# Optimization experiments

Measured on AMD Instinct MI355X. Metric: run time of the kernel, lower is better.

Reference implementation:

```python
import jax, jax.numpy as jnp
import numpy as np

HID, INP = 128, 320
C = HID + INP  # 448


def _fake_quant_w(w):
    # brevitas Int8WeightPerTensorFloat-style symmetric per-tensor fake quant (STE forward)
    scale = jnp.maximum(jnp.max(jnp.abs(w)), 1e-8) / 127.0
    q = jnp.clip(jnp.round(w / scale), -128, 127) * scale
    return w + jax.lax.stop_gradient(q - w)


def _dwconv(x, w, b):
    # depthwise 3x3, SAME padding; w: [C,1,3,3]
    y = jax.lax.conv_general_dilated(x, _fake_quant_w(w), (1, 1), 'SAME',
                                     dimension_numbers=('NCHW', 'OIHW', 'NCHW'),
                                     feature_group_count=x.shape[1])
    return y + b[None, :, None, None]


def _pwconv(x, w, b):
    # pointwise 1x1; w: [O,C,1,1]
    y = jax.lax.conv_general_dilated(x, _fake_quant_w(w), (1, 1), 'SAME',
                                     dimension_numbers=('NCHW', 'OIHW', 'NCHW'))
    return y + b[None, :, None, None]


def setup_inputs() -> dict:
    key = jax.random.key(0)
    ks = jax.random.split(key, 16)
    B, H, W = 8, 64, 128
    d = {
        'h': jax.random.normal(ks[0], (B, HID, H, W), jnp.float32),
        'x': jax.random.normal(ks[1], (B, INP, H, W), jnp.float32),
    }
    i = 2
    for g in ('z', 'r', 'q'):
        d[f'wd{g}'] = jax.random.normal(ks[i], (C, 1, 3, 3), jnp.float32) * 0.1; i += 1
        d[f'bd{g}'] = jax.random.normal(ks[i], (C,), jnp.float32) * 0.01; i += 1
        d[f'wp{g}'] = jax.random.normal(ks[i], (HID, C, 1, 1), jnp.float32) * 0.05; i += 1
        d[f'bp{g}'] = jax.random.normal(ks[i], (HID,), jnp.float32) * 0.01; i += 1
    return d


def reference(h, x, wdz, bdz, wpz, bpz, wdr, bdr, wpr, bpr, wdq, bdq, wpq, bpq):
    hx = jnp.concatenate([h, x], axis=1)  # [B, 448, H, W]
    z = jax.nn.sigmoid(_pwconv(_dwconv(hx, wdz, bdz), wpz, bpz))
    r = jax.nn.sigmoid(_pwconv(_dwconv(hx, wdr, bdr), wpr, bpr))
    rhx = jnp.concatenate([r * h, x], axis=1)
    q = jnp.tanh(_pwconv(_dwconv(rhx, wdq, bdq), wpq, bpq))
    return (1.0 - z) * h + z * q
```

## Files before the change

### kernel.cpp

```cpp
#include <hip/hip_runtime.h>
#include <hip/hip_bf16.h>

#define BB  8
#define HIDC 128
#define INPC 320
#define CC  448
#define HH  64
#define WWI 128
#define HW  8192
#define NT_PER_B 512
#define KG  56

using bf16   = __hip_bfloat16;
using bf16x8 = __attribute__((ext_vector_type(8))) __bf16;
using bf16x4 = __attribute__((ext_vector_type(4))) __bf16;
using bf16x2 = __attribute__((ext_vector_type(2))) __bf16;
using f32x4  = __attribute__((ext_vector_type(4))) float;
using f32x2  = __attribute__((ext_vector_type(2))) float;

__device__ __forceinline__ float b2f(bf16 v) { return __bfloat162float(v); }
__device__ __forceinline__ bf16  f2b(float v) { return __float2bfloat16(v); }

__device__ __forceinline__ void load2(const float* p, float& v0, float& v1) {
  f32x2 t = *reinterpret_cast<const f32x2*>(p);
  v0 = t[0]; v1 = t[1];
}
__device__ __forceinline__ void load2(const bf16* p, float& v0, float& v1) {
  bf16x2 t = *reinterpret_cast<const bf16x2*>(p);
  v0 = (float)t[0]; v1 = (float)t[1];
}

__global__ __launch_bounds__(256) void quant_kernel(
    const float* wdz, const float* wpz, const float* wdr, const float* wpr,
    const float* wdq, const float* wpq, float* qwd, bf16* qwp, float* scales)
{
  const float* src = nullptr; int n = 0; float* df = nullptr; bf16* db = nullptr;
  int sidx = -1;
  switch (blockIdx.x) {
    case 0: src = wdz; n = CC * 9;    df = qwd;                 break;
    case 1: src = wpz; n = HIDC * CC; db = qwp;                 sidx = 0; break;
    case 2: src = wdr; n = CC * 9;    df = qwd + 4096;          break;
    case 3: src = wpr; n = HIDC * CC; db = qwp + HIDC * CC;     sidx = 1; break;
    case 4: src = wdq; n = CC * 9;    df = qwd + 8192;          break;
    case 5: src = wpq; n = HIDC * CC; db = qwp + 2 * HIDC * CC; sidx = 2; break;
  }
  __shared__ float red[256];
  int tid = threadIdx.x;
  float m = 0.f;
  for (int i = tid * 4; i < n; i += 1024) {
    f32x4 v = *reinterpret_cast<const f32x4*>(src + i);
    m = fmaxf(m, fmaxf(fmaxf(fabsf(v[0]), fabsf(v[1])), fmaxf(fabsf(v[2]), fabsf(v[3]))));
  }
  red[tid] = m; __syncthreads();
  for (int s = 128; s > 0; s >>= 1) {
    if (tid < s) red[tid] = fmaxf(red[tid], red[tid + s]);
    __syncthreads();
  }
  float scale = fmaxf(red[0], 1e-8f) / 127.f;
  if (sidx >= 0 && tid == 0) scales[sidx] = scale;
  for (int i = tid * 4; i < n; i += 1024) {
    f32x4 v = *reinterpret_cast<const f32x4*>(src + i);
    float q[4];
#pragma unroll
    for (int j = 0; j < 4; j++) {
      float qq = rintf(v[j] / scale);
      q[j] = fminf(fmaxf(qq, -128.f), 127.f);
    }
    if (df) {
      f32x4 o; o[0] = q[0] * scale; o[1] = q[1] * scale; o[2] = q[2] * scale; o[3] = q[3] * scale;
      *reinterpret_cast<f32x4*>(df + i) = o;
    } else {
      bf16x4 o; o[0] = (__bf16)q[0]; o[1] = (__bf16)q[1]; o[2] = (__bf16)q[2]; o[3] = (__bf16)q[3];
      *reinterpret_cast<bf16x4*>(db + i) = o;
    }
  }
}

template <int NG, typename TH>
__global__ __launch_bounds__(256) void dwconv_kernel(
    const TH*    __restrict__ src_h,
    const float* __restrict__ src_x,
    const float* __restrict__ w0, const float* __restrict__ b0,
    const float* __restrict__ w1, const float* __restrict__ b1,
    bf16* __restrict__ out0, bf16* __restrict__ out1)
{
  int cg   = blockIdx.x;
  int b    = blockIdx.z;
  int lane = threadIdx.x & 63;
  int w    = threadIdx.x >> 6;
  int y    = blockIdx.y * 4 + w;
  int x0   = lane * 2;
  int c0   = cg * 8;
  bool in_h = (c0 < HIDC);
  const TH*    baseh = src_h + ((size_t)b * HIDC + c0) * HW;
  const float* basex = src_x + ((size_t)b * INPC + (c0 - HIDC)) * HW;

  float a0[2][8], a1[2][8];
#pragma unroll
  for (int i = 0; i < 8; i++) {
    int c = c0 + i;
    const TH*    ph = baseh + (size_t)i * HW;
    const float* pf = basex + (size_t)i * HW;
    float s00 = 0.f, s01 = 0.f, s10 = 0.f, s11 = 0.f;
#pragma unroll
    for (int dy = -1; dy <= 1; dy++) {
      int yy = y + dy;
      bool valid = (unsigned)yy < (unsigned)HH;
      int yc = valid ? yy : (yy < 0 ? 0 : HH - 1);
      float v0, v1;
      if (in_h) load2(ph + yc * WWI + x0, v0, v1);
      else      load2(pf + yc * WWI + x0, v0, v1);
      if (!valid) { v0 = v1 = 0.f; }
      float vL = __shfl_up(v1, 1);
      if (lane == 0)  vL = 0.f;
      float vR = __shfl_down(v0, 1);
      if (lane == 63) vR = 0.f;
      int t = (dy + 1) * 3;
      float u0 = w0[c * 9 + t], u1 = w0[c * 9 + t + 1], u2 = w0[c * 9 + t + 2];
      s00 += vL * u0 + v0 * u1 + v1 * u2;
      s01 += v0 * u0 + v1 * u1 + vR * u2;
      if (NG == 2) {
        float q0 = w1[c * 9 + t], q1 = w1[c * 9 + t + 1], q2 = w1[c * 9 + t + 2];
        s10 += vL * q0 + v0 * q1 + v1 * q2;
        s11 += v0 * q0 + v1 * q1 + vR * q2;
      }
    }
    float bb0 = b0[c];
    a0[0][i] = s00 + bb0;
    a0[1][i] = s01 + bb0;
    if (NG == 2) {
      float bb1 = b1[c];
      a1[0][i] = s10 + bb1;
      a1[1][i] = s11 + bb1;
    }
  }

#pragma unroll
  for (int p = 0; p < 2; p++) {
    int px = x0 + p;
    size_t off = (((size_t)b * NT_PER_B + y * 8 + (px >> 4)) * KG + cg) * 128 + (px & 15) * 8;
    bf16x8 v0;
#pragma unroll
    for (int i = 0; i < 8; i++) v0[i] = (__bf16)a0[p][i];
    *reinterpret_cast<bf16x8*>(out0 + off) = v0;
    if (NG == 2) {
      bf16x8 v1;
#pragma unroll
      for (int i = 0; i < 8; i++) v1[i] = (__bf16)a1[p][i];
      *reinterpret_cast<bf16x8*>(out1 + off) = v1;
    }
  }
}

__device__ __forceinline__ void pw_gemm(const bf16* __restrict__ dbt,
                                        const bf16* __restrict__ wpm,
                                        int lane, f32x4 acc[2][4])
{
  int quad = lane >> 4;
  int lr   = lane & 15;
  const bf16* wp0 = wpm + (size_t)lr * CC + quad * 8;
  const bf16* bsrc = dbt + (size_t)lane * 8;
#pragma unroll
  for (int kk = 0; kk < 14; kk++) {
    bf16x8 a0 = *reinterpret_cast<const bf16x8*>(wp0 + kk * 32);
    bf16x8 a1 = *reinterpret_cast<const bf16x8*>(wp0 + 16 * CC + kk * 32);
#pragma unroll
    for (int nf = 0; nf < 4; nf++) {
      bf16x8 bfr = *reinterpret_cast<const bf16x8*>(bsrc + ((size_t)nf * KG + kk * 4) * 128);
      acc[0][nf] = __builtin_amdgcn_mfma_f32_16x16x32_bf16(a0, bfr, acc[0][nf], 0, 0, 0);
      acc[1][nf] = __builtin_amdgcn_mfma_f32_16x16x32_bf16(a1, bfr, acc[1][nf], 0, 0, 0);
    }
  }
}

__global__ __launch_bounds__(256) void pw_zr_kernel(
    const bf16*  __restrict__ dz,
    const bf16*  __restrict__ dr,
    const bf16*  __restrict__ qwp,
    const float* __restrict__ bpz, const float* __restrict__ bpr,
    const float* __restrict__ scales,
    const float* __restrict__ h,
    bf16* __restrict__ zout, bf16* __restrict__ rhout)
{
  int gate = blockIdx.z;
  const bf16*  dbuf = gate ? dr : dz;
  const bf16*  wp   = qwp + (size_t)gate * HIDC * CC;
  const float* bp   = gate ? bpr : bpz;
  float s = scales[gate];

  int b    = blockIdx.y;
  int n0   = blockIdx.x * 64;
  int nt0  = blockIdx.x * 4;
  int wave = threadIdx.x >> 6;
  int lane = threadIdx.x & 63;
  int quad = lane >> 4;
  int lr   = lane & 15;
  int m0   = wave * 32;
  f32x4 acc[2][4] = {};
  const bf16* dbt = dbuf + ((size_t)b * NT_PER_B + nt0) * (KG * 128);

  pw_gemm(dbt, wp + (size_t)m0 * CC, lane, acc);

#pragma unroll
  for (int mf = 0; mf < 2; mf++) {
#pragma unroll
    for (int r = 0; r < 4; r++) {
      int o = m0 + mf * 16 + quad * 4 + r;
      float bias = bp[o];
#pragma unroll
      for (int nf = 0; nf < 4; nf++) {
        int n = n0 + nf * 16 + lr;
        size_t idx = ((size_t)b * HIDC + o) * HW + n;
        float pre = acc[mf][nf][r] * s + bias;
        float sv  = 1.f / (1.f + expf(-pre));
        if (gate == 0) zout[idx]  = f2b(sv);
        else           rhout[idx] = f2b(sv * h[idx]);
      }
    }
  }
}

__global__ __launch_bounds__(256) void pw_q_kernel(
    const bf16*  __restrict__ dbuf,
    const bf16*  __restrict__ wp,
    const float* __restrict__ bp,
    const float* __restrict__ scale_p,
    const float* __restrict__ h,
    const bf16*  __restrict__ zin,
    float* __restrict__ qout)
{
  int b    = blockIdx.y;
  int n0   = blockIdx.x * 64;
  int nt0  = blockIdx.x * 4;
  int wave = threadIdx.x >> 6;
  int lane = threadIdx.x & 63;
  int quad = lane >> 4;
  int lr   = lane & 15;
  int m0   = wave * 32;
  float s = *scale_p;
  f32x4 acc[2][4] = {};
  const bf16* dbt = dbuf + ((size_t)b * NT_PER_B + nt0) * (KG * 128);

  pw_gemm(dbt, wp + (size_t)m0 * CC, lane, acc);

#pragma unroll
  for (int mf = 0; mf < 2; mf++) {
#pragma unroll
    for (int r = 0; r < 4; r++) {
      int o = m0 + mf * 16 + quad * 4 + r;
      float bias = bp[o];
#pragma unroll
      for (int nf = 0; nf < 4; nf++) {
        int n = n0 + nf * 16 + lr;
        size_t idx = ((size_t)b * HIDC + o) * HW + n;
        float pre = acc[mf][nf][r] * s + bias;
        float qv = tanhf(pre);
        float zv = b2f(zin[idx]);
        float hv = h[idx];
        qout[idx] = (1.f - zv) * hv + zv * qv;
      }
    }
  }
}

extern "C" void kernel_launch(void* const* d_in, const int* in_sizes, int n_in,
                              void* d_out, int out_size, void* d_ws, size_t ws_size,
                              hipStream_t stream)
{
  const float* h   = (const float*)d_in[0];
  const float* x   = (const float*)d_in[1];
  const float* wdz = (const float*)d_in[2];
  const float* bdz = (const float*)d_in[3];
  const float* wpz = (const float*)d_in[4];
  const float* bpz = (const float*)d_in[5];
  const float* wdr = (const float*)d_in[6];
  const float* bdr = (const float*)d_in[7];
  const float* wpr = (const float*)d_in[8];
  const float* bpr = (const float*)d_in[9];
  const float* wdq = (const float*)d_in[10];
  const float* bdq = (const float*)d_in[11];
  const float* wpq = (const float*)d_in[12];
  const float* bpq = (const float*)d_in[13];

  char* ws = (char*)d_ws;
  float* qwd    = (float*)ws;
  float* scales = qwd + 12288;
  bf16*  qwp    = (bf16*)(ws + 65536);
  const size_t DBUF_ELEMS = (size_t)BB * NT_PER_B * KG * 128;
  bf16*  dz   = (bf16*)(ws + (1 << 20));
  bf16*  dr   = dz + DBUF_ELEMS;
  bf16*  zbuf = dr + DBUF_ELEMS;
  bf16*  rh   = zbuf + (size_t)BB * HIDC * HW;

  quant_kernel<<<6, 256, 0, stream>>>(wdz, wpz, wdr, wpr, wdq, wpq, qwd, qwp, scales);

  dim3 dgrid(56, 16, 8);
  dwconv_kernel<2, float><<<dgrid, 256, 0, stream>>>(h, x, qwd, bdz, qwd + 4096, bdr, dz, dr);

  dim3 zrgrid(128, 8, 2);
  pw_zr_kernel<<<zrgrid, 256, 0, stream>>>(dz, dr, qwp, bpz, bpr, scales, h, zbuf, rh);

  dwconv_kernel<1, bf16><<<dgrid, 256, 0, stream>>>(rh, x, qwd + 8192, bdq, nullptr, nullptr,
                                                    dz, nullptr);

  dim3 pgrid(128, 8);
  pw_q_kernel<<<pgrid, 256, 0, stream>>>(dz, qwp + 2 * HIDC * CC, bpq, scales + 2, h, zbuf,
                                         (float*)d_out);
}
```

Measured before the change: 410.7 us.

## Fuse depthwise conv into pointwise MFMA GEMM through LDS staging

```diff
diff --git a/kernel.cpp b/kernel.cpp
--- a/kernel.cpp
+++ b/kernel.cpp
@@ -8,27 +8,17 @@
 #define HH  64
 #define WWI 128
 #define HW  8192
-#define NT_PER_B 512
 #define KG  56
 
 using bf16   = __hip_bfloat16;
 using bf16x8 = __attribute__((ext_vector_type(8))) __bf16;
 using bf16x4 = __attribute__((ext_vector_type(4))) __bf16;
-using bf16x2 = __attribute__((ext_vector_type(2))) __bf16;
 using f32x4  = __attribute__((ext_vector_type(4))) float;
-using f32x2  = __attribute__((ext_vector_type(2))) float;
 
 __device__ __forceinline__ float b2f(bf16 v) { return __bfloat162float(v); }
 __device__ __forceinline__ bf16  f2b(float v) { return __float2bfloat16(v); }
-
-__device__ __forceinline__ void load2(const float* p, float& v0, float& v1) {
-  f32x2 t = *reinterpret_cast<const f32x2*>(p);
-  v0 = t[0]; v1 = t[1];
-}
-__device__ __forceinline__ void load2(const bf16* p, float& v0, float& v1) {
-  bf16x2 t = *reinterpret_cast<const bf16x2*>(p);
-  v0 = (float)t[0]; v1 = (float)t[1];
-}
+__device__ __forceinline__ float tof(float v) { return v; }
+__device__ __forceinline__ float tof(bf16 v)  { return __bfloat162float(v); }
 
 __global__ __launch_bounds__(256) void quant_kernel(
     const float* wdz, const float* wpz, const float* wdr, const float* wpr,
@@ -76,188 +66,122 @@
   }
 }
 
-template <int NG, typename TH>
-__global__ __launch_bounds__(256) void dwconv_kernel(
+template <int KIND, typename TH>
+__global__ __launch_bounds__(512) void fused_kernel(
     const TH*    __restrict__ src_h,
     const float* __restrict__ src_x,
-    const float* __restrict__ w0, const float* __restrict__ b0,
-    const float* __restrict__ w1, const float* __restrict__ b1,
-    bf16* __restrict__ out0, bf16* __restrict__ out1)
+    const float* __restrict__ wd_base,
+    const float* __restrict__ bd0, const float* __restrict__ bd1,
+    const bf16*  __restrict__ wp_base,
+    const float* __restrict__ bp0, const float* __restrict__ bp1,
+    const float* __restrict__ scales,
+    const float* __restrict__ h,
+    const bf16*  __restrict__ zin,
+    bf16* __restrict__ zout, bf16* __restrict__ rhout, float* __restrict__ qout)
 {
-  int cg   = blockIdx.x;
-  int b    = blockIdx.z;
+  __shared__ __align__(16) bf16 Blds[4 * KG * 128];
+
+  int gate = (KIND == 0) ? (int)(blockIdx.z >> 3) : 0;
+  int b    = blockIdx.z & 7;
+  int xseg = blockIdx.x;
+  int y    = blockIdx.y;
+  int wid  = threadIdx.x >> 6;
   int lane = threadIdx.x & 63;
-  int w    = threadIdx.x >> 6;
-  int y    = blockIdx.y * 4 + w;
-  int x0   = lane * 2;
-  int c0   = cg * 8;
-  bool in_h = (c0 < HIDC);
-  const TH*    baseh = src_h + ((size_t)b * HIDC + c0) * HW;
-  const float* basex = src_x + ((size_t)b * INPC + (c0 - HIDC)) * HW;
-
-  float a0[2][8], a1[2][8];
-#pragma unroll
-  for (int i = 0; i < 8; i++) {
-    int c = c0 + i;
-    const TH*    ph = baseh + (size_t)i * HW;
-    const float* pf = basex + (size_t)i * HW;
-    float s00 = 0.f, s01 = 0.f, s10 = 0.f, s11 = 0.f;
-#pragma unroll
-    for (int dy = -1; dy <= 1; dy++) {
-      int yy = y + dy;
-      bool valid = (unsigned)yy < (unsigned)HH;
-      int yc = valid ? yy : (yy < 0 ? 0 : HH - 1);
-      float v0, v1;
-      if (in_h) load2(ph + yc * WWI + x0, v0, v1);
-      else      load2(pf + yc * WWI + x0, v0, v1);
-      if (!valid) { v0 = v1 = 0.f; }
-      float vL = __shfl_up(v1, 1);
-      if (lane == 0)  vL = 0.f;
-      float vR = __shfl_down(v0, 1);
-      if (lane == 63) vR = 0.f;
-      int t = (dy + 1) * 3;
-      float u0 = w0[c * 9 + t], u1 = w0[c * 9 + t + 1], u2 = w0[c * 9 + t + 2];
-      s00 += vL * u0 + v0 * u1 + v1 * u2;
-      s01 += v0 * u0 + v1 * u1 + vR * u2;
-      if (NG == 2) {
-        float q0 = w1[c * 9 + t], q1 = w1[c * 9 + t + 1], q2 = w1[c * 9 + t + 2];
-        s10 += vL * q0 + v0 * q1 + v1 * q2;
-        s11 += v0 * q0 + v1 * q1 + vR * q2;
+
+  const float* wd = wd_base + gate * 4096;
+  const float* bd = gate ? bd1 : bd0;
+  const bf16*  wp = wp_base + (size_t)gate * HIDC * CC;
+  const float* bp = gate ? bp1 : bp0;
+  float s = scales[gate];
+
+  int yc[3]; bool vld[3];
+#pragma unroll
+  for (int d = 0; d < 3; d++) {
+    int yy = y + d - 1;
+    vld[d] = (unsigned)yy < (unsigned)HH;
+    yc[d]  = vld[d] ? yy : (yy < 0 ? 0 : HH - 1);
+  }
+
+  int cell = lane >> 4, ln = lane & 15;
+  int cbase = wid * 56;
+  for (int i8 = 0; i8 < 7; i8++) {
+    int c0 = cbase + i8 * 8;
+    bool in_h = (c0 < HIDC);
+    const TH*    ph = src_h + ((size_t)b * HIDC + c0) * HW;
+    const float* pf = src_x + ((size_t)b * INPC + (c0 - HIDC)) * HW;
+    bf16x8 pack;
+#pragma unroll
+    for (int j = 0; j < 8; j++) {
+      int c = c0 + j;
+      float sacc = 0.f;
+#pragma unroll
+      for (int d = 0; d < 3; d++) {
+        float v0, vl, vr;
+        if (in_h) {
+          const TH* rp = ph + (size_t)j * HW + yc[d] * WWI + xseg * 64;
+          v0 = tof(rp[lane]);
+          vl = __shfl_up(v0, 1);
+          if (lane == 0)  vl = xseg ? tof(rp[-1]) : 0.f;
+          vr = __shfl_down(v0, 1);
+          if (lane == 63) vr = xseg ? 0.f : tof(rp[64]);
+        } else {
+          const float* rp = pf + (size_t)j * HW + yc[d] * WWI + xseg * 64;
+          v0 = rp[lane];
+          vl = __shfl_up(v0, 1);
+          if (lane == 0)  vl = xseg ? rp[-1] : 0.f;
+          vr = __shfl_down(v0, 1);
+          if (lane == 63) vr = xseg ? 0.f : rp[64];
+        }
+        if (!vld[d]) { v0 = 0.f; vl = 0.f; vr = 0.f; }
+        int t = c * 9 + d * 3;
+        sacc += vl * wd[t] + v0 * wd[t + 1] + vr * wd[t + 2];
       }
-    }
-    float bb0 = b0[c];
-    a0[0][i] = s00 + bb0;
-    a0[1][i] = s01 + bb0;
-    if (NG == 2) {
-      float bb1 = b1[c];
-      a1[0][i] = s10 + bb1;
-      a1[1][i] = s11 + bb1;
-    }
-  }
-
-#pragma unroll
-  for (int p = 0; p < 2; p++) {
-    int px = x0 + p;
-    size_t off = (((size_t)b * NT_PER_B + y * 8 + (px >> 4)) * KG + cg) * 128 + (px & 15) * 8;
-    bf16x8 v0;
-#pragma unroll
-    for (int i = 0; i < 8; i++) v0[i] = (__bf16)a0[p][i];
-    *reinterpret_cast<bf16x8*>(out0 + off) = v0;
-    if (NG == 2) {
-      bf16x8 v1;
-#pragma unroll
-      for (int i = 0; i < 8; i++) v1[i] = (__bf16)a1[p][i];
-      *reinterpret_cast<bf16x8*>(out1 + off) = v1;
-    }
-  }
-}
-
-__device__ __forceinline__ void pw_gemm(const bf16* __restrict__ dbt,
-                                        const bf16* __restrict__ wpm,
-                                        int lane, f32x4 acc[2][4])
-{
-  int quad = lane >> 4;
-  int lr   = lane & 15;
-  const bf16* wp0 = wpm + (size_t)lr * CC + quad * 8;
-  const bf16* bsrc = dbt + (size_t)lane * 8;
+      pack[j] = (__bf16)(sacc + bd[c]);
+    }
+    int kgg = wid * 7 + i8;
+    *reinterpret_cast<bf16x8*>(&Blds[((size_t)cell * KG + kgg) * 128 + ln * 8]) = pack;
+  }
+  __syncthreads();
+
+  int quad = lane >> 4, lr = lane & 15;
+  int m0  = (wid & 3) * 32;
+  int nc0 = (wid >> 2) * 2;
+  const bf16* bsrc = &Blds[(size_t)nc0 * KG * 128 + lane * 8];
+  const bf16* wp0  = wp + (size_t)(m0 + lr) * CC + quad * 8;
+  f32x4 acc[2][2] = {};
 #pragma unroll
   for (int kk = 0; kk < 14; kk++) {
     bf16x8 a0 = *reinterpret_cast<const bf16x8*>(wp0 + kk * 32);
     bf16x8 a1 = *reinterpret_cast<const bf16x8*>(wp0 + 16 * CC + kk * 32);
 #pragma unroll
-    for (int nf = 0; nf < 4; nf++) {
+    for (int nf = 0; nf < 2; nf++) {
       bf16x8 bfr = *reinterpret_cast<const bf16x8*>(bsrc + ((size_t)nf * KG + kk * 4) * 128);
       acc[0][nf] = __builtin_amdgcn_mfma_f32_16x16x32_bf16(a0, bfr, acc[0][nf], 0, 0, 0);
       acc[1][nf] = __builtin_amdgcn_mfma_f32_16x16x32_bf16(a1, bfr, acc[1][nf], 0, 0, 0);
     }
   }
-}
-
-__global__ __launch_bounds__(256) void pw_zr_kernel(
-    const bf16*  __restrict__ dz,
-    const bf16*  __restrict__ dr,
-    const bf16*  __restrict__ qwp,
-    const float* __restrict__ bpz, const float* __restrict__ bpr,
-    const float* __restrict__ scales,
-    const float* __restrict__ h,
-    bf16* __restrict__ zout, bf16* __restrict__ rhout)
-{
-  int gate = blockIdx.z;
-  const bf16*  dbuf = gate ? dr : dz;
-  const bf16*  wp   = qwp + (size_t)gate * HIDC * CC;
-  const float* bp   = gate ? bpr : bpz;
-  float s = scales[gate];
-
-  int b    = blockIdx.y;
-  int n0   = blockIdx.x * 64;
-  int nt0  = blockIdx.x * 4;
-  int wave = threadIdx.x >> 6;
-  int lane = threadIdx.x & 63;
-  int quad = lane >> 4;
-  int lr   = lane & 15;
-  int m0   = wave * 32;
-  f32x4 acc[2][4] = {};
-  const bf16* dbt = dbuf + ((size_t)b * NT_PER_B + nt0) * (KG * 128);
-
-  pw_gemm(dbt, wp + (size_t)m0 * CC, lane, acc);
 
 #pragma unroll
   for (int mf = 0; mf < 2; mf++) {
 #pragma unroll
-    for (int r = 0; r < 4; r++) {
-      int o = m0 + mf * 16 + quad * 4 + r;
+    for (int rr = 0; rr < 4; rr++) {
+      int o = m0 + mf * 16 + quad * 4 + rr;
       float bias = bp[o];
 #pragma unroll
-      for (int nf = 0; nf < 4; nf++) {
-        int n = n0 + nf * 16 + lr;
-        size_t idx = ((size_t)b * HIDC + o) * HW + n;
-        float pre = acc[mf][nf][r] * s + bias;
-        float sv  = 1.f / (1.f + expf(-pre));
-        if (gate == 0) zout[idx]  = f2b(sv);
-        else           rhout[idx] = f2b(sv * h[idx]);
-      }
-    }
-  }
-}
-
-__global__ __launch_bounds__(256) void pw_q_kernel(
-    const bf16*  __restrict__ dbuf,
-    const bf16*  __restrict__ wp,
-    const float* __restrict__ bp,
-    const float* __restrict__ scale_p,
-    const float* __restrict__ h,
-    const bf16*  __restrict__ zin,
-    float* __restrict__ qout)
-{
-  int b    = blockIdx.y;
-  int n0   = blockIdx.x * 64;
-  int nt0  = blockIdx.x * 4;
-  int wave = threadIdx.x >> 6;
-  int lane = threadIdx.x & 63;
-  int quad = lane >> 4;
-  int lr   = lane & 15;
-  int m0   = wave * 32;
-  float s = *scale_p;
-  f32x4 acc[2][4] = {};
-  const bf16* dbt = dbuf + ((size_t)b * NT_PER_B + nt0) * (KG * 128);
-
-  pw_gemm(dbt, wp + (size_t)m0 * CC, lane, acc);
-
-#pragma unroll
-  for (int mf = 0; mf < 2; mf++) {
-#pragma unroll
-    for (int r = 0; r < 4; r++) {
-      int o = m0 + mf * 16 + quad * 4 + r;
-      float bias = bp[o];
-#pragma unroll
-      for (int nf = 0; nf < 4; nf++) {
-        int n = n0 + nf * 16 + lr;
-        size_t idx = ((size_t)b * HIDC + o) * HW + n;
-        float pre = acc[mf][nf][r] * s + bias;
-        float qv = tanhf(pre);
-        float zv = b2f(zin[idx]);
-        float hv = h[idx];
-        qout[idx] = (1.f - zv) * hv + zv * qv;
+      for (int nf = 0; nf < 2; nf++) {
+        int n = xseg * 64 + (wid >> 2) * 32 + nf * 16 + lr;
+        size_t idx = ((size_t)b * HIDC + o) * HW + y * WWI + n;
+        float pre = acc[mf][nf][rr] * s + bias;
+        if (KIND == 0) {
+          float sv = 1.f / (1.f + expf(-pre));
+          if (gate == 0) zout[idx]  = f2b(sv);
+          else           rhout[idx] = f2b(sv * h[idx]);
+        } else {
+          float qv = tanhf(pre);
+          float zv = b2f(zin[idx]);
+          float hv = h[idx];
+          qout[idx] = (1.f - zv) * hv + zv * qv;
+        }
       }
     }
   }
@@ -286,24 +210,16 @@
   float* qwd    = (float*)ws;
   float* scales = qwd + 12288;
   bf16*  qwp    = (bf16*)(ws + 65536);
-  const size_t DBUF_ELEMS = (size_t)BB * NT_PER_B * KG * 128;
-  bf16*  dz   = (bf16*)(ws + (1 << 20));
-  bf16*  dr   = dz + DBUF_ELEMS;
-  bf16*  zbuf = dr + DBUF_ELEMS;
-  bf16*  rh   = zbuf + (size_t)BB * HIDC * HW;
+  bf16*  zbuf   = (bf16*)(ws + (1 << 20));
+  bf16*  rh     = zbuf + (size_t)BB * HIDC * HW;
 
   quant_kernel<<<6, 256, 0, stream>>>(wdz, wpz, wdr, wpr, wdq, wpq, qwd, qwp, scales);
 
-  dim3 dgrid(56, 16, 8);
-  dwconv_kernel<2, float><<<dgrid, 256, 0, stream>>>(h, x, qwd, bdz, qwd + 4096, bdr, dz, dr);
-
-  dim3 zrgrid(128, 8, 2);
-  pw_zr_kernel<<<zrgrid, 256, 0, stream>>>(dz, dr, qwp, bpz, bpr, scales, h, zbuf, rh);
-
-  dwconv_kernel<1, bf16><<<dgrid, 256, 0, stream>>>(rh, x, qwd + 8192, bdq, nullptr, nullptr,
-                                                    dz, nullptr);
-
-  dim3 pgrid(128, 8);
-  pw_q_kernel<<<pgrid, 256, 0, stream>>>(dz, qwp + 2 * HIDC * CC, bpq, scales + 2, h, zbuf,
-                                         (float*)d_out);
+  fused_kernel<0, float><<<dim3(2, 64, 16), 512, 0, stream>>>(
+      h, x, qwd, bdz, bdr, qwp, bpz, bpr, scales, h, nullptr,
+      zbuf, rh, nullptr);
+
+  fused_kernel<1, bf16><<<dim3(2, 64, 8), 512, 0, stream>>>(
+      rh, x, qwd + 8192, bdq, nullptr, qwp + 2 * HIDC * CC, bpq, nullptr,
+      scales + 2, h, zbuf, nullptr, nullptr, (float*)d_out);
 }
```

Result: slower. 1.451 ms (+253.3%).
